# Kernel tuning notes

Hardware: AMD Instinct MI355X
Metric: run time of the kernel (lower is better)

Reference implementation:

```python
import jax, jax.numpy as jnp
import numpy as np

N = 100_000      # num nodes
E = 600_000      # num edges (before self-loops)
IN, H, C, OUT = 128, 4, 64, 1   # in_channels, heads, hidden_channels, out_channels
NEG_SLOPE = 0.2  # PyG GATConv leaky_relu slope


def setup_inputs() -> dict:
    key = jax.random.key(0)
    ks = jax.random.split(key, 12)
    init = lambda k, sh: (jax.random.normal(k, sh, jnp.float32) * 0.05)
    return {
        "x": jax.random.normal(ks[0], (N, IN), jnp.float32),
        "edge_index": jax.random.randint(ks[1], (2, E), 0, N, dtype=jnp.int32),
        # conv1: GATConv(IN -> C, heads=H, concat) -> out dim H*C
        "W1": init(ks[2], (IN, H, C)),
        "att_src1": init(ks[3], (H, C)),
        "att_dst1": init(ks[4], (H, C)),
        "b1": jnp.zeros((H * C,), jnp.float32),
        # conv2: GATConv(H*C -> C, heads=H, head-mean to match Linear(C, OUT))
        "W2": init(ks[5], (H * C, H, C)),
        "att_src2": init(ks[6], (H, C)),
        "att_dst2": init(ks[7], (H, C)),
        "b2": jnp.zeros((C,), jnp.float32),
        # PReLU (single shared parameter, torch default init 0.25)
        "prelu_a": jnp.float32(0.25),
        # level_predictor: Linear(C, OUT)
        "Wl": init(ks[8], (C, OUT)),
        "bl": jnp.zeros((OUT,), jnp.float32),
    }


def _add_self_loops(edge_index):
    loops = jnp.arange(N, dtype=edge_index.dtype)
    return jnp.concatenate([edge_index, jnp.stack([loops, loops])], axis=1)


def _gat_conv(x, src, dst, W, att_src, att_dst, bias, concat):
    # x: [N, F]; W: [F, H, C]
    h = jnp.einsum("nf,fhc->nhc", x, W)                      # [N, H, C]
    a_src = jnp.sum(h * att_src, axis=-1)                     # [N, H]
    a_dst = jnp.sum(h * att_dst, axis=-1)                     # [N, H]
    e = jax.nn.leaky_relu(a_src[src] + a_dst[dst], NEG_SLOPE)  # [Etot, H]
    # segment-softmax over incoming edges of each destination node
    m = jax.ops.segment_max(e, dst, num_segments=N)            # [N, H]
    e = jnp.exp(e - m[dst])
    denom = jax.ops.segment_sum(e, dst, num_segments=N)        # [N, H]
    alpha = e / (denom[dst] + 1e-16)                           # [Etot, H]
    out = jax.ops.segment_sum(h[src] * alpha[..., None], dst, num_segments=N)  # [N, H, C]
    out = out.reshape(N, H * C) if concat else out.mean(axis=1)
    return out + bias


def _prelu(x, a):
    return jnp.where(x >= 0, x, a * x)


def reference(x, edge_index, W1, att_src1, att_dst1, b1,
              W2, att_src2, att_dst2, b2, prelu_a, Wl, bl):
    # k-hop 'extraction' over the full node set is an identity -> full edge set.
    ei = _add_self_loops(edge_index)
    src, dst = ei[0], ei[1]
    h = _gat_conv(x, src, dst, W1, att_src1, att_dst1, b1, concat=True)   # [N, H*C]
    h = _prelu(h, prelu_a)
    h = _gat_conv(h, src, dst, W2, att_src2, att_dst2, b2, concat=False)  # [N, C]
    h = _prelu(h, prelu_a)
    return (h @ Wl + bl).squeeze(-1)                                       # [N]
```

## Files before the change

kernel.cpp:

```cpp
#include <hip/hip_runtime.h>
#include <cstdint>
#include <cstddef>

static constexpr int N_NODES = 100000;
static constexpr int N_EDGES = 600000;
static constexpr int E_TOT   = N_EDGES + N_NODES;
static constexpr float NEG_SLOPE = 0.2f;

typedef __attribute__((ext_vector_type(8))) _Float16 f16x8;
typedef __attribute__((ext_vector_type(4))) float f32x4;
typedef __attribute__((ext_vector_type(4))) _Float16 half4;

__device__ __forceinline__ float leaky(float x) { return x >= 0.f ? x : NEG_SLOPE * x; }

__device__ __forceinline__ void gload16(const void* g, void* l) {
  __builtin_amdgcn_global_load_lds(
      (const __attribute__((address_space(1))) unsigned int*)g,
      (__attribute__((address_space(3))) unsigned int*)l,
      16, 0, 0);
}


__global__ __launch_bounds__(256) void k_init_counts(int* __restrict__ counts) {
  int i = blockIdx.x * 256 + threadIdx.x;
  if (i < N_NODES) counts[i] = 1;
}

__global__ __launch_bounds__(256) void k_hist(const int* __restrict__ ei, int* __restrict__ counts) {
  int e = blockIdx.x * 256 + threadIdx.x;
  if (e < N_EDGES) atomicAdd(&counts[ei[N_EDGES + e]], 1);
}

__global__ __launch_bounds__(256) void k_scan1(const int* __restrict__ counts,
                                               int* __restrict__ partial,
                                               int* __restrict__ blockSums) {
  __shared__ int tmp[256];
  int tid = threadIdx.x;
  int i = blockIdx.x * 256 + tid;
  int v = (i < N_NODES) ? counts[i] : 0;
  tmp[tid] = v;
  __syncthreads();
  for (int off = 1; off < 256; off <<= 1) {
    int t = (tid >= off) ? tmp[tid - off] : 0;
    __syncthreads();
    tmp[tid] += t;
    __syncthreads();
  }
  if (i < N_NODES) partial[i] = tmp[tid] - v;
  if (tid == 255) blockSums[blockIdx.x] = tmp[tid];
}

__global__ __launch_bounds__(512) void k_scan2(int* __restrict__ blockSums, int nb) {
  __shared__ int tmp[512];
  int tid = threadIdx.x;
  int v = (tid < nb) ? blockSums[tid] : 0;
  tmp[tid] = v;
  __syncthreads();
  for (int off = 1; off < 512; off <<= 1) {
    int t = (tid >= off) ? tmp[tid - off] : 0;
    __syncthreads();
    tmp[tid] += t;
    __syncthreads();
  }
  if (tid < nb) blockSums[tid] = tmp[tid] - v;
}

__global__ __launch_bounds__(256) void k_scan3(const int* __restrict__ partial,
                                               const int* __restrict__ blockSums,
                                               int* __restrict__ rowptr,
                                               int* __restrict__ fill) {
  int i = blockIdx.x * 256 + threadIdx.x;
  if (i < N_NODES) {
    int v = partial[i] + blockSums[blockIdx.x];
    rowptr[i] = v;
    fill[i] = v;
  }
  if (i == 0) rowptr[N_NODES] = E_TOT;
}

__global__ __launch_bounds__(256) void k_scatter(const int* __restrict__ ei,
                                                 int* __restrict__ fill,
                                                 int* __restrict__ esrc) {
  int i = blockIdx.x * 256 + threadIdx.x;
  if (i >= E_TOT) return;
  int s, d;
  if (i < N_EDGES) { s = ei[i]; d = ei[N_EDGES + i]; }
  else             { s = i - N_EDGES; d = s; }
  int pos = atomicAdd(&fill[d], 1);
  esrc[pos] = s;
}


template <int K>
__global__ __launch_bounds__(256) void k_wconv(const float* __restrict__ W,
                                               _Float16* __restrict__ Wt) {
  int t = blockIdx.x * 256 + threadIdx.x;
  if (t >= K * 256) return;
  int k = t >> 8, c = t & 255;
  Wt[(size_t)c * K + k] = (_Float16)W[t];
}

template <int K>
__global__ __launch_bounds__(256) void k_wa(const float* __restrict__ W,
                                            const float* __restrict__ att_s,
                                            const float* __restrict__ att_d,
                                            _Float16* __restrict__ Wat) {
  int k = blockIdx.x;
  int h = threadIdx.x >> 6, c = threadIdx.x & 63;
  float wv = W[(size_t)k * 256 + h * 64 + c];
  float ps = wv * att_s[h * 64 + c];
  float pd = wv * att_d[h * 64 + c];
#pragma unroll
  for (int off = 32; off > 0; off >>= 1) {
    ps += __shfl_xor(ps, off);
    pd += __shfl_xor(pd, off);
  }
  if (c == 0) {
    Wat[(size_t)h * K + k] = (_Float16)ps;
    Wat[(size_t)(4 + h) * K + k] = (_Float16)pd;
  }
  if (threadIdx.x >= 8 && threadIdx.x < 16)
    Wat[(size_t)threadIdx.x * K + k] = (_Float16)0.f;
}


__global__ __launch_bounds__(256) void k_conv_x(const float* __restrict__ X,
                                                _Float16* __restrict__ X16) {
  size_t t = (size_t)blockIdx.x * 256 + threadIdx.x;
  float4 v = *(const float4*)&X[t * 4];
  half4 o;
  o[0] = (_Float16)v.x; o[1] = (_Float16)v.y;
  o[2] = (_Float16)v.z; o[3] = (_Float16)v.w;
  *(half4*)&X16[t * 4] = o;
}


template <int K>
__global__ __launch_bounds__(256, 3) void k_gemm_mfma(
    const _Float16* __restrict__ A, const _Float16* __restrict__ B,
    const _Float16* __restrict__ Wa,
    _Float16* __restrict__ H, float* __restrict__ asrc, float* __restrict__ adst) {
  __shared__ __align__(16) _Float16 lds[2][10240];

  const int tid = threadIdx.x;
  const int w = tid >> 6, lane = tid & 63;
  const int lhi = lane >> 4, llo = lane & 15;
  const int wrow = blockIdx.x * 64;
  const int wcol = w * 64;

  const int sr = tid >> 2;
  const int sc = (tid & 3) ^ (sr & 3);
  int ar = wrow + sr; if (ar > N_NODES - 1) ar = N_NODES - 1;
  const _Float16* gA  = &A[(size_t)ar * K + sc * 8];
  const _Float16* gB0 = &B[(size_t)(0 * 64 + sr) * K + sc * 8];
  const _Float16* gB1 = &B[(size_t)(1 * 64 + sr) * K + sc * 8];
  const _Float16* gB2 = &B[(size_t)(2 * 64 + sr) * K + sc * 8];
  const _Float16* gB3 = &B[(size_t)(3 * 64 + sr) * K + sc * 8];
  const int wb = w * 512;

  const _Float16* gW = &Wa[(size_t)llo * K + lhi * 8];

  f32x4 acc[4][4] = {};
  f32x4 acca[4] = {};

  const int ach = (lhi ^ (llo & 3)) * 8;

  auto STAGE = [&](int buf, int kc) {
    _Float16* L = lds[buf];
    gload16(gA + kc,  L + 0    + wb);
    gload16(gB0 + kc, L + 2048 + wb);
    gload16(gB1 + kc, L + 4096 + wb);
    gload16(gB2 + kc, L + 6144 + wb);
    gload16(gB3 + kc, L + 8192 + wb);
  };

  STAGE(0, 0);
  __syncthreads();

  constexpr int NT = K / 32;
  int cur = 0;
#pragma unroll 2
  for (int t = 0; t < NT; ++t) {
    if (t + 1 < NT) STAGE(cur ^ 1, (t + 1) * 32);

    f16x8 wfrag{};
    if (w == 0) wfrag = *(const f16x8*)&gW[t * 32];

    const _Float16* L = lds[cur];
    f16x8 af[4], bf[4];
#pragma unroll
    for (int rt = 0; rt < 4; ++rt)
      af[rt] = *(const f16x8*)&L[(rt * 16 + llo) * 32 + ach];
#pragma unroll
    for (int ct = 0; ct < 4; ++ct)
      bf[ct] = *(const f16x8*)&L[2048 + (wcol + ct * 16 + llo) * 32 + ach];

#pragma unroll
    for (int ct = 0; ct < 4; ++ct)
#pragma unroll
      for (int rt = 0; rt < 4; ++rt)
        acc[rt][ct] = __builtin_amdgcn_mfma_f32_16x16x32_f16(af[rt], bf[ct], acc[rt][ct], 0, 0, 0);
    if (w == 0) {
#pragma unroll
      for (int rt = 0; rt < 4; ++rt)
        acca[rt] = __builtin_amdgcn_mfma_f32_16x16x32_f16(af[rt], wfrag, acca[rt], 0, 0, 0);
    }
    __syncthreads();
    cur ^= 1;
  }

#pragma unroll
  for (int rt = 0; rt < 4; ++rt) {
    const int r0 = wrow + rt * 16 + lhi * 4;
#pragma unroll
    for (int ct = 0; ct < 4; ++ct) {
      const int cc = wcol + ct * 16 + llo;
#pragma unroll
      for (int e = 0; e < 4; ++e) {
        int r = r0 + e;
        if (r < N_NODES) H[(size_t)r * 256 + cc] = (_Float16)acc[rt][ct][e];
      }
    }
    if (w == 0 && llo < 8) {
#pragma unroll
      for (int e = 0; e < 4; ++e) {
        int r = r0 + e;
        if (r < N_NODES) {
          float v = acca[rt][e];
          if (llo < 4) asrc[(size_t)r * 4 + llo] = v;
          else         adst[(size_t)r * 4 + (llo - 4)] = v;
        }
      }
    }
  }
}


__global__ __launch_bounds__(256) void k_stats(const float4* __restrict__ asrc4,
                                               const float4* __restrict__ adst4,
                                               const int* __restrict__ rowptr,
                                               const int* __restrict__ esrc,
                                               float4* __restrict__ pbuf4,
                                               float4* __restrict__ dinv4) {
  int d = blockIdx.x * 256 + threadIdx.x;
  if (d >= N_NODES) return;
  const int beg = rowptr[d], end = rowptr[d + 1];
  const float4 ad = adst4[d];

  float4 den = make_float4(0.f, 0.f, 0.f, 0.f);
  for (int j = beg; j < end; ++j) {
    const float4 a = asrc4[esrc[j]];
    float4 p;
    p.x = __expf(leaky(a.x + ad.x));
    p.y = __expf(leaky(a.y + ad.y));
    p.z = __expf(leaky(a.z + ad.z));
    p.w = __expf(leaky(a.w + ad.w));
    den.x += p.x; den.y += p.y; den.z += p.z; den.w += p.w;
    pbuf4[j] = p;
  }
  float4 di;
  di.x = 1.f / (den.x + 1e-16f);
  di.y = 1.f / (den.y + 1e-16f);
  di.z = 1.f / (den.z + 1e-16f);
  di.w = 1.f / (den.w + 1e-16f);
  dinv4[d] = di;
}


__device__ __forceinline__ float4 gather_rows(const _Float16* __restrict__ htab,
                                              const float* __restrict__ pbuf,
                                              const int* __restrict__ esrc,
                                              int beg, int end, int lane, int myh) {
  float4 acc = make_float4(0.f, 0.f, 0.f, 0.f);
  for (int w = beg; w < end; w += 8) {
    const int cnt = end - w;
    const float pl = pbuf[(size_t)w * 4 + (lane & 31)];
    const int   sl = esrc[w + (lane & 7)];
    int   s[8];
    float p[8];
#pragma unroll
    for (int i = 0; i < 8; ++i) {
      s[i] = __shfl(sl, i);
      p[i] = __shfl(pl, i * 4 + myh);
    }
#pragma unroll
    for (int i = 1; i < 8; ++i) {
      if (i >= cnt) { s[i] = s[0]; p[i] = 0.f; }
    }
    half4 v[8];
#pragma unroll
    for (int i = 0; i < 8; ++i)
      v[i] = *(const half4*)&htab[(size_t)s[i] * 256 + 4 * lane];
#pragma unroll
    for (int i = 0; i < 8; ++i) {
      acc.x = fmaf(p[i], (float)v[i][0], acc.x);
      acc.y = fmaf(p[i], (float)v[i][1], acc.y);
      acc.z = fmaf(p[i], (float)v[i][2], acc.z);
      acc.w = fmaf(p[i], (float)v[i][3], acc.w);
    }
  }
  return acc;
}


__global__ __launch_bounds__(256) void k_agg1(const _Float16* __restrict__ h1,
                                              const float* __restrict__ pbuf,
                                              const float* __restrict__ dinv,
                                              const int* __restrict__ rowptr,
                                              const int* __restrict__ esrc,
                                              const float* __restrict__ b1,
                                              const float* __restrict__ prelu_a,
                                              _Float16* __restrict__ outp) {
  int gid = blockIdx.x * 256 + threadIdx.x;
  int dst = gid >> 6;
  int lane = threadIdx.x & 63;
  if (dst >= N_NODES) return;
  const int beg = rowptr[dst], end = rowptr[dst + 1];
  const int myh = lane >> 4;

  float4 acc = gather_rows(h1, pbuf, esrc, beg, end, lane, myh);
  const float sc = dinv[(size_t)dst * 4 + myh];
  acc.x *= sc; acc.y *= sc; acc.z *= sc; acc.w *= sc;

  const float a = prelu_a[0];
  const int c = 4 * lane;
  const float4 bv = *(const float4*)&b1[c];
  float4 r;
  r.x = acc.x + bv.x; r.x = r.x >= 0.f ? r.x : a * r.x;
  r.y = acc.y + bv.y; r.y = r.y >= 0.f ? r.y : a * r.y;
  r.z = acc.z + bv.z; r.z = r.z >= 0.f ? r.z : a * r.z;
  r.w = acc.w + bv.w; r.w = r.w >= 0.f ? r.w : a * r.w;

  half4 o;
  o[0] = (_Float16)r.x; o[1] = (_Float16)r.y;
  o[2] = (_Float16)r.z; o[3] = (_Float16)r.w;
  *(half4*)&outp[(size_t)dst * 256 + c] = o;
}


__global__ __launch_bounds__(256) void k_agg2(const _Float16* __restrict__ h2,
                                              const float* __restrict__ pbuf,
                                              const float* __restrict__ dinv,
                                              const int* __restrict__ rowptr,
                                              const int* __restrict__ esrc,
                                              const float* __restrict__ b2,
                                              const float* __restrict__ prelu_a,
                                              const float* __restrict__ Wl,
                                              const float* __restrict__ bl,
                                              float* __restrict__ out) {
  int gid = blockIdx.x * 256 + threadIdx.x;
  int dst = gid >> 6;
  int lane = threadIdx.x & 63;
  if (dst >= N_NODES) return;
  const int beg = rowptr[dst], end = rowptr[dst + 1];
  const int myh = lane >> 4;

  float4 acc = gather_rows(h2, pbuf, esrc, beg, end, lane, myh);
  const float sc = dinv[(size_t)dst * 4 + myh];
  acc.x *= sc; acc.y *= sc; acc.z *= sc; acc.w *= sc;

#pragma unroll
  for (int off = 16; off < 64; off <<= 1) {
    acc.x += __shfl_xor(acc.x, off);
    acc.y += __shfl_xor(acc.y, off);
    acc.z += __shfl_xor(acc.z, off);
    acc.w += __shfl_xor(acc.w, off);
  }

  const float a = prelu_a[0];
  const int c0 = 4 * (lane & 15);
  float4 v;
  v.x = 0.25f * acc.x + b2[c0 + 0]; v.x = v.x >= 0.f ? v.x : a * v.x;
  v.y = 0.25f * acc.y + b2[c0 + 1]; v.y = v.y >= 0.f ? v.y : a * v.y;
  v.z = 0.25f * acc.z + b2[c0 + 2]; v.z = v.z >= 0.f ? v.z : a * v.z;
  v.w = 0.25f * acc.w + b2[c0 + 3]; v.w = v.w >= 0.f ? v.w : a * v.w;

  float p = v.x * Wl[c0 + 0] + v.y * Wl[c0 + 1] + v.z * Wl[c0 + 2] + v.w * Wl[c0 + 3];
#pragma unroll
  for (int off = 1; off < 16; off <<= 1) p += __shfl_xor(p, off);

  if (lane == 0) out[dst] = p + bl[0];
}


static inline int cdiv(int a, int b) { return (a + b - 1) / b; }

extern "C" void kernel_launch(void* const* d_in, const int* in_sizes, int n_in,
                              void* d_out, int out_size, void* d_ws, size_t ws_size,
                              hipStream_t stream) {
  const float* x   = (const float*)d_in[0];
  const int*   ei  = (const int*)d_in[1];
  const float* W1  = (const float*)d_in[2];
  const float* as1 = (const float*)d_in[3];
  const float* ad1 = (const float*)d_in[4];
  const float* b1  = (const float*)d_in[5];
  const float* W2  = (const float*)d_in[6];
  const float* as2 = (const float*)d_in[7];
  const float* ad2 = (const float*)d_in[8];
  const float* b2  = (const float*)d_in[9];
  const float* pa  = (const float*)d_in[10];
  const float* Wl  = (const float*)d_in[11];
  const float* bl  = (const float*)d_in[12];
  float* out = (float*)d_out;

  char* ws = (char*)d_ws;
  size_t off = 0;
  auto alloc = [&](size_t bytes) -> void* {
    void* p = ws + off;
    off += (bytes + 255) & ~(size_t)255;
    return p;
  };

  _Float16* hbufA = (_Float16*)alloc((size_t)N_NODES * 256 * sizeof(_Float16));
  _Float16* R1 = (_Float16*)alloc((size_t)N_NODES * 256 * sizeof(_Float16));
  _Float16* x16  = R1;
  _Float16* h1p  = R1;

  float* asrc1 = (float*)alloc((size_t)N_NODES * 4 * sizeof(float));
  float* adst1 = (float*)alloc((size_t)N_NODES * 4 * sizeof(float));
  float* asrc2 = (float*)alloc((size_t)N_NODES * 4 * sizeof(float));
  float* adst2 = (float*)alloc((size_t)N_NODES * 4 * sizeof(float));
  float* pbuf  = (float*)alloc(((size_t)E_TOT * 4 + 64) * sizeof(float));
  float* dinv  = (float*)alloc((size_t)N_NODES * 4 * sizeof(float));

  _Float16* Wt1  = (_Float16*)alloc(256 * 128 * sizeof(_Float16));
  _Float16* Wat1 = (_Float16*)alloc(16 * 128 * sizeof(_Float16));
  _Float16* Wt2  = (_Float16*)alloc(256 * 256 * sizeof(_Float16));
  _Float16* Wat2 = (_Float16*)alloc(16 * 256 * sizeof(_Float16));

  int* counts  = (int*)alloc((size_t)N_NODES * sizeof(int));
  int* partial = (int*)alloc((size_t)N_NODES * sizeof(int));
  int* rowptr  = (int*)alloc((size_t)(N_NODES + 1) * sizeof(int));
  int* fill    = (int*)alloc((size_t)N_NODES * sizeof(int));
  int* esrc    = (int*)alloc(((size_t)E_TOT + 64) * sizeof(int));
  int* blockSums = (int*)alloc(2048 * sizeof(int));

  const int NB = cdiv(N_NODES, 256);

  k_init_counts<<<NB, 256, 0, stream>>>(counts);
  k_hist<<<cdiv(N_EDGES, 256), 256, 0, stream>>>(ei, counts);
  k_scan1<<<NB, 256, 0, stream>>>(counts, partial, blockSums);
  k_scan2<<<1, 512, 0, stream>>>(blockSums, NB);
  k_scan3<<<NB, 256, 0, stream>>>(partial, blockSums, rowptr, fill);
  k_scatter<<<cdiv(E_TOT, 256), 256, 0, stream>>>(ei, fill, esrc);

  k_wconv<128><<<cdiv(128 * 256, 256), 256, 0, stream>>>(W1, Wt1);
  k_wa<128><<<128, 256, 0, stream>>>(W1, as1, ad1, Wat1);
  k_wconv<256><<<cdiv(256 * 256, 256), 256, 0, stream>>>(W2, Wt2);
  k_wa<256><<<256, 256, 0, stream>>>(W2, as2, ad2, Wat2);

  k_conv_x<<<N_NODES * 128 / 4 / 256, 256, 0, stream>>>(x, x16);

  const int GEMM_GRID = cdiv(N_NODES, 64);

  k_gemm_mfma<128><<<GEMM_GRID, 256, 0, stream>>>(x16, Wt1, Wat1, hbufA, asrc1, adst1);
  k_stats<<<NB, 256, 0, stream>>>((const float4*)asrc1, (const float4*)adst1,
                                  rowptr, esrc, (float4*)pbuf, (float4*)dinv);
  k_agg1<<<N_NODES * 64 / 256, 256, 0, stream>>>(hbufA, pbuf, dinv, rowptr, esrc,
                                                 b1, pa, h1p);

  k_gemm_mfma<256><<<GEMM_GRID, 256, 0, stream>>>(h1p, Wt2, Wat2, hbufA, asrc2, adst2);
  k_stats<<<NB, 256, 0, stream>>>((const float4*)asrc2, (const float4*)adst2,
                                  rowptr, esrc, (float4*)pbuf, (float4*)dinv);
  k_agg2<<<N_NODES * 64 / 256, 256, 0, stream>>>(hbufA, pbuf, dinv, rowptr, esrc,
                                                 b2, pa, Wl, bl, out);
}
```

Before: 296.2 us.

## Pad CSR rows to multiples of eight and pre-normalize attention weights

The CSR row layout is padded so each destination's edge list is a multiple of 8. The stats kernel fills padding slots with a dummy source and zero weight. The stats kernel now makes two passes, computing the softmax denominator first and then writing normalized alpha, so the aggregation kernels no longer read dinv or handle partial tail masking. This trades recomputing exp and asrc gathers in k_stats, plus extra padded gather work in the aggregations, for simpler branch-free inner loops.

```diff
diff --git a/kernel.cpp b/kernel.cpp
--- a/kernel.cpp
+++ b/kernel.cpp
@@ -5,6 +5,7 @@
 static constexpr int N_NODES = 100000;
 static constexpr int N_EDGES = 600000;
 static constexpr int E_TOT   = N_EDGES + N_NODES;
+static constexpr int E_PAD_MAX = E_TOT + 7 * N_NODES + 64;
 static constexpr float NEG_SLOPE = 0.2f;
 
 typedef __attribute__((ext_vector_type(8))) _Float16 f16x8;
@@ -37,7 +38,7 @@
   __shared__ int tmp[256];
   int tid = threadIdx.x;
   int i = blockIdx.x * 256 + tid;
-  int v = (i < N_NODES) ? counts[i] : 0;
+  int v = (i < N_NODES) ? ((counts[i] + 7) & ~7) : 0;
   tmp[tid] = v;
   __syncthreads();
   for (int off = 1; off < 256; off <<= 1) {
@@ -67,27 +68,28 @@
 
 __global__ __launch_bounds__(256) void k_scan3(const int* __restrict__ partial,
                                                const int* __restrict__ blockSums,
-                                               int* __restrict__ rowptr,
+                                               const int* __restrict__ counts,
+                                               int* __restrict__ rowptr2,
                                                int* __restrict__ fill) {
   int i = blockIdx.x * 256 + threadIdx.x;
   if (i < N_NODES) {
     int v = partial[i] + blockSums[blockIdx.x];
-    rowptr[i] = v;
+    rowptr2[i] = v;
     fill[i] = v;
-  }
-  if (i == 0) rowptr[N_NODES] = E_TOT;
+    if (i == N_NODES - 1) rowptr2[N_NODES] = v + ((counts[i] + 7) & ~7);
+  }
 }
 
 __global__ __launch_bounds__(256) void k_scatter(const int* __restrict__ ei,
                                                  int* __restrict__ fill,
-                                                 int* __restrict__ esrc) {
+                                                 int* __restrict__ esrcP) {
   int i = blockIdx.x * 256 + threadIdx.x;
   if (i >= E_TOT) return;
   int s, d;
   if (i < N_EDGES) { s = ei[i]; d = ei[N_EDGES + i]; }
   else             { s = i - N_EDGES; d = s; }
   int pos = atomicAdd(&fill[d], 1);
-  esrc[pos] = s;
+  esrcP[pos] = s;
 }
 
 
@@ -238,54 +240,62 @@
 
 __global__ __launch_bounds__(256) void k_stats(const float4* __restrict__ asrc4,
                                                const float4* __restrict__ adst4,
-                                               const int* __restrict__ rowptr,
-                                               const int* __restrict__ esrc,
-                                               float4* __restrict__ pbuf4,
-                                               float4* __restrict__ dinv4) {
+                                               const int* __restrict__ rowptr2,
+                                               const int* __restrict__ counts,
+                                               int* __restrict__ esrcP,
+                                               float4* __restrict__ pbuf4) {
   int d = blockIdx.x * 256 + threadIdx.x;
   if (d >= N_NODES) return;
-  const int beg = rowptr[d], end = rowptr[d + 1];
+  const int beg = rowptr2[d];
+  const int deg = counts[d];
   const float4 ad = adst4[d];
 
   float4 den = make_float4(0.f, 0.f, 0.f, 0.f);
-  for (int j = beg; j < end; ++j) {
-    const float4 a = asrc4[esrc[j]];
-    float4 p;
-    p.x = __expf(leaky(a.x + ad.x));
-    p.y = __expf(leaky(a.y + ad.y));
-    p.z = __expf(leaky(a.z + ad.z));
-    p.w = __expf(leaky(a.w + ad.w));
-    den.x += p.x; den.y += p.y; den.z += p.z; den.w += p.w;
-    pbuf4[j] = p;
+  for (int j = 0; j < deg; ++j) {
+    const float4 a = asrc4[esrcP[beg + j]];
+    den.x += __expf(leaky(a.x + ad.x));
+    den.y += __expf(leaky(a.y + ad.y));
+    den.z += __expf(leaky(a.z + ad.z));
+    den.w += __expf(leaky(a.w + ad.w));
   }
   float4 di;
   di.x = 1.f / (den.x + 1e-16f);
   di.y = 1.f / (den.y + 1e-16f);
   di.z = 1.f / (den.z + 1e-16f);
   di.w = 1.f / (den.w + 1e-16f);
-  dinv4[d] = di;
+
+  for (int j = 0; j < deg; ++j) {
+    const float4 a = asrc4[esrcP[beg + j]];
+    float4 p;
+    p.x = __expf(leaky(a.x + ad.x)) * di.x;
+    p.y = __expf(leaky(a.y + ad.y)) * di.y;
+    p.z = __expf(leaky(a.z + ad.z)) * di.z;
+    p.w = __expf(leaky(a.w + ad.w)) * di.w;
+    pbuf4[beg + j] = p;
+  }
+
+  const int padend = beg + ((deg + 7) & ~7);
+  const int s0 = esrcP[beg];
+  for (int j = beg + deg; j < padend; ++j) {
+    esrcP[j] = s0;
+    pbuf4[j] = make_float4(0.f, 0.f, 0.f, 0.f);
+  }
 }
 
 
 __device__ __forceinline__ float4 gather_rows(const _Float16* __restrict__ htab,
                                               const float* __restrict__ pbuf,
-                                              const int* __restrict__ esrc,
+                                              const int* __restrict__ esrcP,
                                               int beg, int end, int lane, int myh) {
   float4 acc = make_float4(0.f, 0.f, 0.f, 0.f);
   for (int w = beg; w < end; w += 8) {
-    const int cnt = end - w;
-    const float pl = pbuf[(size_t)w * 4 + (lane & 31)];
-    const int   sl = esrc[w + (lane & 7)];
-    int   s[8];
+    const int sl = esrcP[w + (lane & 7)];
+    int s[8];
     float p[8];
 #pragma unroll
     for (int i = 0; i < 8; ++i) {
       s[i] = __shfl(sl, i);
-      p[i] = __shfl(pl, i * 4 + myh);
-    }
-#pragma unroll
-    for (int i = 1; i < 8; ++i) {
-      if (i >= cnt) { s[i] = s[0]; p[i] = 0.f; }
+      p[i] = pbuf[(size_t)(w + i) * 4 + myh];
     }
     half4 v[8];
 #pragma unroll
@@ -305,9 +315,8 @@
 
 __global__ __launch_bounds__(256) void k_agg1(const _Float16* __restrict__ h1,
                                               const float* __restrict__ pbuf,
-                                              const float* __restrict__ dinv,
-                                              const int* __restrict__ rowptr,
-                                              const int* __restrict__ esrc,
+                                              const int* __restrict__ rowptr2,
+                                              const int* __restrict__ esrcP,
                                               const float* __restrict__ b1,
                                               const float* __restrict__ prelu_a,
                                               _Float16* __restrict__ outp) {
@@ -315,12 +324,10 @@
   int dst = gid >> 6;
   int lane = threadIdx.x & 63;
   if (dst >= N_NODES) return;
-  const int beg = rowptr[dst], end = rowptr[dst + 1];
+  const int beg = rowptr2[dst], end = rowptr2[dst + 1];
   const int myh = lane >> 4;
 
-  float4 acc = gather_rows(h1, pbuf, esrc, beg, end, lane, myh);
-  const float sc = dinv[(size_t)dst * 4 + myh];
-  acc.x *= sc; acc.y *= sc; acc.z *= sc; acc.w *= sc;
+  float4 acc = gather_rows(h1, pbuf, esrcP, beg, end, lane, myh);
 
   const float a = prelu_a[0];
   const int c = 4 * lane;
@@ -340,9 +347,8 @@
 
 __global__ __launch_bounds__(256) void k_agg2(const _Float16* __restrict__ h2,
                                               const float* __restrict__ pbuf,
-                                              const float* __restrict__ dinv,
-                                              const int* __restrict__ rowptr,
-                                              const int* __restrict__ esrc,
+                                              const int* __restrict__ rowptr2,
+                                              const int* __restrict__ esrcP,
                                               const float* __restrict__ b2,
                                               const float* __restrict__ prelu_a,
                                               const float* __restrict__ Wl,
@@ -352,12 +358,10 @@
   int dst = gid >> 6;
   int lane = threadIdx.x & 63;
   if (dst >= N_NODES) return;
-  const int beg = rowptr[dst], end = rowptr[dst + 1];
+  const int beg = rowptr2[dst], end = rowptr2[dst + 1];
   const int myh = lane >> 4;
 
-  float4 acc = gather_rows(h2, pbuf, esrc, beg, end, lane, myh);
-  const float sc = dinv[(size_t)dst * 4 + myh];
-  acc.x *= sc; acc.y *= sc; acc.z *= sc; acc.w *= sc;
+  float4 acc = gather_rows(h2, pbuf, esrcP, beg, end, lane, myh);
 
 #pragma unroll
   for (int off = 16; off < 64; off <<= 1) {
@@ -420,8 +424,8 @@
   float* adst1 = (float*)alloc((size_t)N_NODES * 4 * sizeof(float));
   float* asrc2 = (float*)alloc((size_t)N_NODES * 4 * sizeof(float));
   float* adst2 = (float*)alloc((size_t)N_NODES * 4 * sizeof(float));
-  float* pbuf  = (float*)alloc(((size_t)E_TOT * 4 + 64) * sizeof(float));
-  float* dinv  = (float*)alloc((size_t)N_NODES * 4 * sizeof(float));
+  float* pbuf  = (float*)alloc((size_t)E_PAD_MAX * 4 * sizeof(float));
+  int*   esrcP = (int*)alloc((size_t)E_PAD_MAX * sizeof(int));
 
   _Float16* Wt1  = (_Float16*)alloc(256 * 128 * sizeof(_Float16));
   _Float16* Wat1 = (_Float16*)alloc(16 * 128 * sizeof(_Float16));
@@ -430,9 +434,8 @@
 
   int* counts  = (int*)alloc((size_t)N_NODES * sizeof(int));
   int* partial = (int*)alloc((size_t)N_NODES * sizeof(int));
-  int* rowptr  = (int*)alloc((size_t)(N_NODES + 1) * sizeof(int));
+  int* rowptr2 = (int*)alloc((size_t)(N_NODES + 1) * sizeof(int));
   int* fill    = (int*)alloc((size_t)N_NODES * sizeof(int));
-  int* esrc    = (int*)alloc(((size_t)E_TOT + 64) * sizeof(int));
   int* blockSums = (int*)alloc(2048 * sizeof(int));
 
   const int NB = cdiv(N_NODES, 256);
@@ -441,8 +444,8 @@
   k_hist<<<cdiv(N_EDGES, 256), 256, 0, stream>>>(ei, counts);
   k_scan1<<<NB, 256, 0, stream>>>(counts, partial, blockSums);
   k_scan2<<<1, 512, 0, stream>>>(blockSums, NB);
-  k_scan3<<<NB, 256, 0, stream>>>(partial, blockSums, rowptr, fill);
-  k_scatter<<<cdiv(E_TOT, 256), 256, 0, stream>>>(ei, fill, esrc);
+  k_scan3<<<NB, 256, 0, stream>>>(partial, blockSums, counts, rowptr2, fill);
+  k_scatter<<<cdiv(E_TOT, 256), 256, 0, stream>>>(ei, fill, esrcP);
 
   k_wconv<128><<<cdiv(128 * 256, 256), 256, 0, stream>>>(W1, Wt1);
   k_wa<128><<<128, 256, 0, stream>>>(W1, as1, ad1, Wat1);
@@ -455,13 +458,13 @@
 
   k_gemm_mfma<128><<<GEMM_GRID, 256, 0, stream>>>(x16, Wt1, Wat1, hbufA, asrc1, adst1);
   k_stats<<<NB, 256, 0, stream>>>((const float4*)asrc1, (const float4*)adst1,
-                                  rowptr, esrc, (float4*)pbuf, (float4*)dinv);
-  k_agg1<<<N_NODES * 64 / 256, 256, 0, stream>>>(hbufA, pbuf, dinv, rowptr, esrc,
+                                  rowptr2, counts, esrcP, (float4*)pbuf);
+  k_agg1<<<N_NODES * 64 / 256, 256, 0, stream>>>(hbufA, pbuf, rowptr2, esrcP,
                                                  b1, pa, h1p);
 
   k_gemm_mfma<256><<<GEMM_GRID, 256, 0, stream>>>(h1p, Wt2, Wat2, hbufA, asrc2, adst2);
   k_stats<<<NB, 256, 0, stream>>>((const float4*)asrc2, (const float4*)adst2,
-                                  rowptr, esrc, (float4*)pbuf, (float4*)dinv);
-  k_agg2<<<N_NODES * 64 / 256, 256, 0, stream>>>(hbufA, pbuf, dinv, rowptr, esrc,
+                                  rowptr2, counts, esrcP, (float4*)pbuf);
+  k_agg2<<<N_NODES * 64 / 256, 256, 0, stream>>>(hbufA, pbuf, rowptr2, esrcP,
                                                  b2, pa, Wl, bl, out);
 }
```

After: 316.4 us. +6.8%, slower.

## Fuse softmax stats into aggregation and merge small prep kernels

Applied to the files above, without the earlier changes.

Removes the separate per-node softmax-stats kernel and its edge-sized pbuf buffer. Each aggregation wave now computes the softmax denominator itself and recomputes the edge exponentials while gathering rows. The self-loop edges are written in the scan kernel, the count-init kernel becomes a memset, and the weight and input conversion kernels are merged into two launches. The GEMM launch bound rises to four blocks per CU. Together these cut launches and global traffic, at the cost of extra exp work and extra asrc gathers in the aggregation.

```diff
diff --git a/kernel.cpp b/kernel.cpp
--- a/kernel.cpp
+++ b/kernel.cpp
@@ -20,11 +20,6 @@
       16, 0, 0);
 }
 
-
-__global__ __launch_bounds__(256) void k_init_counts(int* __restrict__ counts) {
-  int i = blockIdx.x * 256 + threadIdx.x;
-  if (i < N_NODES) counts[i] = 1;
-}
 
 __global__ __launch_bounds__(256) void k_hist(const int* __restrict__ ei, int* __restrict__ counts) {
   int e = blockIdx.x * 256 + threadIdx.x;
@@ -37,7 +32,7 @@
   __shared__ int tmp[256];
   int tid = threadIdx.x;
   int i = blockIdx.x * 256 + tid;
-  int v = (i < N_NODES) ? counts[i] : 0;
+  int v = (i < N_NODES) ? counts[i] + 1 : 0;
   tmp[tid] = v;
   __syncthreads();
   for (int off = 1; off < 256; off <<= 1) {
@@ -68,12 +63,14 @@
 __global__ __launch_bounds__(256) void k_scan3(const int* __restrict__ partial,
                                                const int* __restrict__ blockSums,
                                                int* __restrict__ rowptr,
-                                               int* __restrict__ fill) {
+                                               int* __restrict__ fill,
+                                               int* __restrict__ esrc) {
   int i = blockIdx.x * 256 + threadIdx.x;
   if (i < N_NODES) {
     int v = partial[i] + blockSums[blockIdx.x];
     rowptr[i] = v;
-    fill[i] = v;
+    fill[i] = v + 1;
+    esrc[v] = i;
   }
   if (i == 0) rowptr[N_NODES] = E_TOT;
 }
@@ -82,34 +79,56 @@
                                                  int* __restrict__ fill,
                                                  int* __restrict__ esrc) {
   int i = blockIdx.x * 256 + threadIdx.x;
-  if (i >= E_TOT) return;
-  int s, d;
-  if (i < N_EDGES) { s = ei[i]; d = ei[N_EDGES + i]; }
-  else             { s = i - N_EDGES; d = s; }
+  if (i >= N_EDGES) return;
+  int s = ei[i], d = ei[N_EDGES + i];
   int pos = atomicAdd(&fill[d], 1);
   esrc[pos] = s;
 }
 
 
-template <int K>
-__global__ __launch_bounds__(256) void k_wconv(const float* __restrict__ W,
-                                               _Float16* __restrict__ Wt) {
-  int t = blockIdx.x * 256 + threadIdx.x;
-  if (t >= K * 256) return;
-  int k = t >> 8, c = t & 255;
-  Wt[(size_t)c * K + k] = (_Float16)W[t];
-}
-
-template <int K>
-__global__ __launch_bounds__(256) void k_wa(const float* __restrict__ W,
-                                            const float* __restrict__ att_s,
-                                            const float* __restrict__ att_d,
-                                            _Float16* __restrict__ Wat) {
-  int k = blockIdx.x;
+static constexpr int XB = N_NODES * 128 / 4 / 256;
+
+__global__ __launch_bounds__(256) void k_prep(const float* __restrict__ X,
+                                              _Float16* __restrict__ X16,
+                                              const float* __restrict__ W1,
+                                              _Float16* __restrict__ Wt1,
+                                              const float* __restrict__ W2,
+                                              _Float16* __restrict__ Wt2) {
+  int b = blockIdx.x;
+  if (b < XB) {
+    size_t t = (size_t)b * 256 + threadIdx.x;
+    float4 v = *(const float4*)&X[t * 4];
+    half4 o;
+    o[0] = (_Float16)v.x; o[1] = (_Float16)v.y;
+    o[2] = (_Float16)v.z; o[3] = (_Float16)v.w;
+    *(half4*)&X16[t * 4] = o;
+  } else if (b < XB + 128) {
+    int t = (b - XB) * 256 + threadIdx.x;
+    int k = t >> 8, c = t & 255;
+    Wt1[(size_t)c * 128 + k] = (_Float16)W1[t];
+  } else {
+    int t = (b - XB - 128) * 256 + threadIdx.x;
+    int k = t >> 8, c = t & 255;
+    Wt2[(size_t)c * 256 + k] = (_Float16)W2[t];
+  }
+}
+
+__global__ __launch_bounds__(256) void k_wa(const float* __restrict__ W1,
+                                            const float* __restrict__ as1,
+                                            const float* __restrict__ ad1,
+                                            _Float16* __restrict__ Wat1,
+                                            const float* __restrict__ W2,
+                                            const float* __restrict__ as2,
+                                            const float* __restrict__ ad2,
+                                            _Float16* __restrict__ Wat2) {
+  int b = blockIdx.x;
+  const float *W, *as, *adp; _Float16* Wat; int K, k;
+  if (b < 128) { W = W1; as = as1; adp = ad1; Wat = Wat1; K = 128; k = b; }
+  else         { W = W2; as = as2; adp = ad2; Wat = Wat2; K = 256; k = b - 128; }
   int h = threadIdx.x >> 6, c = threadIdx.x & 63;
   float wv = W[(size_t)k * 256 + h * 64 + c];
-  float ps = wv * att_s[h * 64 + c];
-  float pd = wv * att_d[h * 64 + c];
+  float ps = wv * as[h * 64 + c];
+  float pd = wv * adp[h * 64 + c];
 #pragma unroll
   for (int off = 32; off > 0; off >>= 1) {
     ps += __shfl_xor(ps, off);
@@ -124,19 +143,8 @@
 }
 
 
-__global__ __launch_bounds__(256) void k_conv_x(const float* __restrict__ X,
-                                                _Float16* __restrict__ X16) {
-  size_t t = (size_t)blockIdx.x * 256 + threadIdx.x;
-  float4 v = *(const float4*)&X[t * 4];
-  half4 o;
-  o[0] = (_Float16)v.x; o[1] = (_Float16)v.y;
-  o[2] = (_Float16)v.z; o[3] = (_Float16)v.w;
-  *(half4*)&X16[t * 4] = o;
-}
-
-
 template <int K>
-__global__ __launch_bounds__(256, 3) void k_gemm_mfma(
+__global__ __launch_bounds__(256, 4) void k_gemm_mfma(
     const _Float16* __restrict__ A, const _Float16* __restrict__ B,
     const _Float16* __restrict__ Wa,
     _Float16* __restrict__ H, float* __restrict__ asrc, float* __restrict__ adst) {
@@ -236,61 +244,42 @@
 }
 
 
-__global__ __launch_bounds__(256) void k_stats(const float4* __restrict__ asrc4,
-                                               const float4* __restrict__ adst4,
-                                               const int* __restrict__ rowptr,
-                                               const int* __restrict__ esrc,
-                                               float4* __restrict__ pbuf4,
-                                               float4* __restrict__ dinv4) {
-  int d = blockIdx.x * 256 + threadIdx.x;
-  if (d >= N_NODES) return;
-  const int beg = rowptr[d], end = rowptr[d + 1];
-  const float4 ad = adst4[d];
-
-  float4 den = make_float4(0.f, 0.f, 0.f, 0.f);
-  for (int j = beg; j < end; ++j) {
-    const float4 a = asrc4[esrc[j]];
-    float4 p;
-    p.x = __expf(leaky(a.x + ad.x));
-    p.y = __expf(leaky(a.y + ad.y));
-    p.z = __expf(leaky(a.z + ad.z));
-    p.w = __expf(leaky(a.w + ad.w));
-    den.x += p.x; den.y += p.y; den.z += p.z; den.w += p.w;
-    pbuf4[j] = p;
-  }
-  float4 di;
-  di.x = 1.f / (den.x + 1e-16f);
-  di.y = 1.f / (den.y + 1e-16f);
-  di.z = 1.f / (den.z + 1e-16f);
-  di.w = 1.f / (den.w + 1e-16f);
-  dinv4[d] = di;
-}
-
-
-__device__ __forceinline__ float4 gather_rows(const _Float16* __restrict__ htab,
-                                              const float* __restrict__ pbuf,
-                                              const int* __restrict__ esrc,
-                                              int beg, int end, int lane, int myh) {
+__device__ __forceinline__ float4 agg_core(const _Float16* __restrict__ htab,
+                                           const float* __restrict__ asrc,
+                                           const float* __restrict__ adst,
+                                           const int* __restrict__ esrc,
+                                           int dst, int beg, int end,
+                                           int lane, int myh) {
+  const float ad = adst[(size_t)dst * 4 + myh];
+
+  float den = 0.f;
+  for (int j = beg + (lane & 15); j < end; j += 16)
+    den += __expf(leaky(asrc[(size_t)esrc[j] * 4 + myh] + ad));
+#pragma unroll
+  for (int off = 1; off < 16; off <<= 1) den += __shfl_xor(den, off);
+  const float di = 1.f / (den + 1e-16f);
+
   float4 acc = make_float4(0.f, 0.f, 0.f, 0.f);
   for (int w = beg; w < end; w += 8) {
     const int cnt = end - w;
-    const float pl = pbuf[(size_t)w * 4 + (lane & 31)];
-    const int   sl = esrc[w + (lane & 7)];
-    int   s[8];
-    float p[8];
-#pragma unroll
-    for (int i = 0; i < 8; ++i) {
-      s[i] = __shfl(sl, i);
-      p[i] = __shfl(pl, i * 4 + myh);
-    }
-#pragma unroll
-    for (int i = 1; i < 8; ++i) {
-      if (i >= cnt) { s[i] = s[0]; p[i] = 0.f; }
-    }
+    const int sl = esrc[w + (lane & 7)];
+    int s[8];
+#pragma unroll
+    for (int i = 0; i < 8; ++i) s[i] = __shfl(sl, i);
+#pragma unroll
+    for (int i = 1; i < 8; ++i) if (i >= cnt) s[i] = s[0];
+    float av[8];
+#pragma unroll
+    for (int i = 0; i < 8; ++i) av[i] = asrc[(size_t)s[i] * 4 + myh];
     half4 v[8];
 #pragma unroll
     for (int i = 0; i < 8; ++i)
       v[i] = *(const half4*)&htab[(size_t)s[i] * 256 + 4 * lane];
+    float p[8];
+    p[0] = __expf(leaky(av[0] + ad)) * di;
+#pragma unroll
+    for (int i = 1; i < 8; ++i)
+      p[i] = (i < cnt) ? __expf(leaky(av[i] + ad)) * di : 0.f;
 #pragma unroll
     for (int i = 0; i < 8; ++i) {
       acc.x = fmaf(p[i], (float)v[i][0], acc.x);
@@ -304,8 +293,8 @@
 
 
 __global__ __launch_bounds__(256) void k_agg1(const _Float16* __restrict__ h1,
-                                              const float* __restrict__ pbuf,
-                                              const float* __restrict__ dinv,
+                                              const float* __restrict__ asrc,
+                                              const float* __restrict__ adst,
                                               const int* __restrict__ rowptr,
                                               const int* __restrict__ esrc,
                                               const float* __restrict__ b1,
@@ -318,9 +307,7 @@
   const int beg = rowptr[dst], end = rowptr[dst + 1];
   const int myh = lane >> 4;
 
-  float4 acc = gather_rows(h1, pbuf, esrc, beg, end, lane, myh);
-  const float sc = dinv[(size_t)dst * 4 + myh];
-  acc.x *= sc; acc.y *= sc; acc.z *= sc; acc.w *= sc;
+  float4 acc = agg_core(h1, asrc, adst, esrc, dst, beg, end, lane, myh);
 
   const float a = prelu_a[0];
   const int c = 4 * lane;
@@ -339,8 +326,8 @@
 
 
 __global__ __launch_bounds__(256) void k_agg2(const _Float16* __restrict__ h2,
-                                              const float* __restrict__ pbuf,
-                                              const float* __restrict__ dinv,
+                                              const float* __restrict__ asrc,
+                                              const float* __restrict__ adst,
                                               const int* __restrict__ rowptr,
                                               const int* __restrict__ esrc,
                                               const float* __restrict__ b2,
@@ -355,9 +342,7 @@
   const int beg = rowptr[dst], end = rowptr[dst + 1];
   const int myh = lane >> 4;
 
-  float4 acc = gather_rows(h2, pbuf, esrc, beg, end, lane, myh);
-  const float sc = dinv[(size_t)dst * 4 + myh];
-  acc.x *= sc; acc.y *= sc; acc.z *= sc; acc.w *= sc;
+  float4 acc = agg_core(h2, asrc, adst, esrc, dst, beg, end, lane, myh);
 
 #pragma unroll
   for (int off = 16; off < 64; off <<= 1) {
@@ -420,8 +405,6 @@
   float* adst1 = (float*)alloc((size_t)N_NODES * 4 * sizeof(float));
   float* asrc2 = (float*)alloc((size_t)N_NODES * 4 * sizeof(float));
   float* adst2 = (float*)alloc((size_t)N_NODES * 4 * sizeof(float));
-  float* pbuf  = (float*)alloc(((size_t)E_TOT * 4 + 64) * sizeof(float));
-  float* dinv  = (float*)alloc((size_t)N_NODES * 4 * sizeof(float));
 
   _Float16* Wt1  = (_Float16*)alloc(256 * 128 * sizeof(_Float16));
   _Float16* Wat1 = (_Float16*)alloc(16 * 128 * sizeof(_Float16));
@@ -437,31 +420,23 @@
 
   const int NB = cdiv(N_NODES, 256);
 
-  k_init_counts<<<NB, 256, 0, stream>>>(counts);
+  hipMemsetAsync(counts, 0, (size_t)N_NODES * sizeof(int), stream);
   k_hist<<<cdiv(N_EDGES, 256), 256, 0, stream>>>(ei, counts);
   k_scan1<<<NB, 256, 0, stream>>>(counts, partial, blockSums);
   k_scan2<<<1, 512, 0, stream>>>(blockSums, NB);
-  k_scan3<<<NB, 256, 0, stream>>>(partial, blockSums, rowptr, fill);
-  k_scatter<<<cdiv(E_TOT, 256), 256, 0, stream>>>(ei, fill, esrc);
-
-  k_wconv<128><<<cdiv(128 * 256, 256), 256, 0, stream>>>(W1, Wt1);
-  k_wa<128><<<128, 256, 0, stream>>>(W1, as1, ad1, Wat1);
-  k_wconv<256><<<cdiv(256 * 256, 256), 256, 0, stream>>>(W2, Wt2);
-  k_wa<256><<<256, 256, 0, stream>>>(W2, as2, ad2, Wat2);
-
-  k_conv_x<<<N_NODES * 128 / 4 / 256, 256, 0, stream>>>(x, x16);
+  k_scan3<<<NB, 256, 0, stream>>>(partial, blockSums, rowptr, fill, esrc);
+  k_scatter<<<cdiv(N_EDGES, 256), 256, 0, stream>>>(ei, fill, esrc);
+
+  k_prep<<<XB + 128 + 256, 256, 0, stream>>>(x, x16, W1, Wt1, W2, Wt2);
+  k_wa<<<128 + 256, 256, 0, stream>>>(W1, as1, ad1, Wat1, W2, as2, ad2, Wat2);
 
   const int GEMM_GRID = cdiv(N_NODES, 64);
 
   k_gemm_mfma<128><<<GEMM_GRID, 256, 0, stream>>>(x16, Wt1, Wat1, hbufA, asrc1, adst1);
-  k_stats<<<NB, 256, 0, stream>>>((const float4*)asrc1, (const float4*)adst1,
-                                  rowptr, esrc, (float4*)pbuf, (float4*)dinv);
-  k_agg1<<<N_NODES * 64 / 256, 256, 0, stream>>>(hbufA, pbuf, dinv, rowptr, esrc,
+  k_agg1<<<N_NODES * 64 / 256, 256, 0, stream>>>(hbufA, asrc1, adst1, rowptr, esrc,
                                                  b1, pa, h1p);
 
   k_gemm_mfma<256><<<GEMM_GRID, 256, 0, stream>>>(h1p, Wt2, Wat2, hbufA, asrc2, adst2);
-  k_stats<<<NB, 256, 0, stream>>>((const float4*)asrc2, (const float4*)adst2,
-                                  rowptr, esrc, (float4*)pbuf, (float4*)dinv);
-  k_agg2<<<N_NODES * 64 / 256, 256, 0, stream>>>(hbufA, pbuf, dinv, rowptr, esrc,
+  k_agg2<<<N_NODES * 64 / 256, 256, 0, stream>>>(hbufA, asrc2, adst2, rowptr, esrc,
                                                  b2, pa, Wl, bl, out);
 }
```

After: 311.8 us. +5.3%, slower.
